# Performance work log

Hardware: AMD Instinct MI355X
Metric: run time of the kernel (lower is better)

Reference implementation:

```python
import jax, jax.numpy as jnp
import numpy as np

B, N, P, K = 64, 64, 128, 16

def setup_inputs() -> dict:
    key = jax.random.key(0)
    k1, k2, k3, k4 = jax.random.split(key, 4)
    x = jax.random.normal(k1, (B, N, P), dtype=jnp.float32)
    idx = jax.random.randint(k2, (B, P), 0, K)
    x_mask = jax.nn.one_hot(idx, K, dtype=jnp.float32)  # [B, P, K] one-hot
    # xavier_normal_ init for weights [K, N*N]
    std = float(np.sqrt(2.0 / (K + N * N)))
    weights = std * jax.random.normal(k3, (K, N * N), dtype=jnp.float32)
    g = jax.random.uniform(k4, (N * N, N * N), dtype=jnp.float32)
    return {"x": x, "x_mask": x_mask, "weights": weights, "g": g}

def reference(x, x_mask, weights, g):
    b, n, p = x.shape
    wg = jnp.matmul(weights ** 2, g)               # [K, N*N]
    w = jnp.einsum('bpk,km->bpm', x_mask, wg)      # [B, P, N*N]
    ef = jnp.exp(-w.reshape(b, p, n, n))           # [B, P, N, N]
    # torch does x[b].reshape(p, -1, 1): row-major reinterpretation of [N,P] -> [P,N]
    xr = x.reshape(b, p, n)                        # [B, P, N]
    Z = jnp.einsum('bpij,bpj->bi', ef, xr)         # batched matvec, summed over p
    return (Z, w)
```

## Files before the change

kernel.cpp:

```cpp
#include <hip/hip_runtime.h>
#include <hip/hip_bf16.h>


__global__ __launch_bounds__(256) void k_gemm(const float* __restrict__ W,
                                              const float* __restrict__ G,
                                              float* __restrict__ part) {
    __shared__ float  w2[16][256];
    __shared__ float4 red[8 * 256];
    const int tc  = blockIdx.x & 15;
    const int mg  = blockIdx.x >> 4;
    const int tid = threadIdx.x;
    const int tt  = tid >> 4;
    const int col = tid & 15;
    const int t0  = tc * 256;

#pragma unroll
    for (int k = 0; k < 16; ++k) {
        float v = W[k * 4096 + t0 + tid];
        w2[k][tid] = v * v;
    }
    __syncthreads();

    const float4* G4 = (const float4*)G;
    const int mq = mg * 16 + col;

    float4 acc[16];
#pragma unroll
    for (int k = 0; k < 16; ++k) acc[k] = make_float4(0.f, 0.f, 0.f, 0.f);

#pragma unroll 8
    for (int i = 0; i < 16; ++i) {
        const int tl = tt * 16 + i;
        const float4 g4 = G4[(size_t)(t0 + tl) * 1024 + mq];
#pragma unroll
        for (int k = 0; k < 16; ++k) {
            const float s = w2[k][tl];
            acc[k].x = fmaf(s, g4.x, acc[k].x);
            acc[k].y = fmaf(s, g4.y, acc[k].y);
            acc[k].z = fmaf(s, g4.z, acc[k].z);
            acc[k].w = fmaf(s, g4.w, acc[k].w);
        }
    }

    float4* p4 = (float4*)part;
#pragma unroll
    for (int r = 0; r < 2; ++r) {
#pragma unroll
        for (int ks = 0; ks < 8; ++ks)
            red[ks * 256 + tid] = acc[r * 8 + ks];
        __syncthreads();
        if (tid < 128) {
            const int ks = tid >> 4;
            const int c2 = tid & 15;
            float4 s = make_float4(0.f, 0.f, 0.f, 0.f);
#pragma unroll
            for (int t2 = 0; t2 < 16; ++t2) {
                float4 v = red[ks * 256 + t2 * 16 + c2];
                s.x += v.x; s.y += v.y; s.z += v.z; s.w += v.w;
            }
            const int k = r * 8 + ks;
            p4[(size_t)tc * 16384 + (size_t)k * 1024 + mg * 16 + c2] = s;
        }
        __syncthreads();
    }
}

__global__ __launch_bounds__(256) void k_reduce(const float* __restrict__ part,
                                                float* __restrict__ wg,
                                                float* __restrict__ E) {
    const int q = blockIdx.x * 256 + threadIdx.x;
    const float4* p4 = (const float4*)part;
    float4 s = make_float4(0.f, 0.f, 0.f, 0.f);
#pragma unroll
    for (int tc = 0; tc < 16; ++tc) {
        float4 v = p4[(size_t)tc * 16384 + q];
        s.x += v.x; s.y += v.y; s.z += v.z; s.w += v.w;
    }
    ((float4*)wg)[q] = s;
    ((float4*)E)[q] = make_float4(expf(-s.x), expf(-s.y), expf(-s.z), expf(-s.w));
}

__global__ __launch_bounds__(256) void k_wz(const float* __restrict__ x,
                                            const float* __restrict__ xmask,
                                            const float* __restrict__ wg,
                                            const float* __restrict__ E,
                                            float* __restrict__ wout,
                                            float* __restrict__ zout) {
    __shared__ float sw[4][16][64];
    __shared__ int   idx[128];
    __shared__ float zr[16][16];
    const int tid = threadIdx.x;

    if (blockIdx.x < 8192) {
        const int bp = blockIdx.x;
        const float* xm = xmask + (size_t)bp * 16;
        int k = 0;
#pragma unroll
        for (int i = 0; i < 16; ++i) k = (xm[i] > 0.5f) ? i : k;
        const float4* src = (const float4*)(wg + (size_t)k * 4096);
        float4*       dst = (float4*)(wout + (size_t)bp * 4096);
#pragma unroll
        for (int c = 0; c < 4; ++c)
            dst[c * 256 + tid] = src[c * 256 + tid];
        return;
    }

    const int zb = blockIdx.x - 8192;
    const int b  = zb >> 2;
    const int iq = zb & 3;
    const int wv = tid >> 6;
    const int ln = tid & 63;

    if (tid < 128) {
        const float* xm = xmask + ((size_t)b * 128 + tid) * 16;
        int k = 0;
#pragma unroll
        for (int i = 0; i < 16; ++i) k = (xm[i] > 0.5f) ? i : k;
        idx[tid] = k;
    }
#pragma unroll
    for (int c = 0; c < 16; ++c)
        ((float*)sw)[c * 256 + tid] = 0.f;
    __syncthreads();

    const float* xb = x + (size_t)b * 8192;
    for (int p = wv * 32; p < wv * 32 + 32; ++p) {
        int k = idx[p];
        sw[wv][k][ln] += xb[p * 64 + ln];
    }
    __syncthreads();

    for (int e = tid; e < 1024; e += 256) {
        int k2 = e >> 6, j = e & 63;
        sw[0][k2][j] = sw[0][k2][j] + sw[1][k2][j] + sw[2][k2][j] + sw[3][k2][j];
    }
    __syncthreads();

    {
        const int k  = tid >> 4;
        const int il = tid & 15;
        const int i  = iq * 16 + il;
        float a = 0.f;
        const float4* Er = (const float4*)(E + (size_t)k * 4096 + i * 64);
        const float4* sr = (const float4*)(&sw[0][k][0]);
#pragma unroll
        for (int j4 = 0; j4 < 16; ++j4) {
            float4 e4 = Er[j4];
            float4 s4 = sr[j4];
            a = fmaf(e4.x, s4.x, a);
            a = fmaf(e4.y, s4.y, a);
            a = fmaf(e4.z, s4.z, a);
            a = fmaf(e4.w, s4.w, a);
        }
        zr[k][il] = a;
    }
    __syncthreads();
    if (tid < 16) {
        float s = 0.f;
#pragma unroll
        for (int k = 0; k < 16; ++k) s += zr[k][tid];
        zout[b * 64 + iq * 16 + tid] = s;
    }
}

extern "C" void kernel_launch(void* const* d_in, const int* in_sizes, int n_in,
                              void* d_out, int out_size, void* d_ws, size_t ws_size,
                              hipStream_t stream) {
    const float* x     = (const float*)d_in[0];
    const float* xmask = (const float*)d_in[1];
    const float* W     = (const float*)d_in[2];
    const float* G     = (const float*)d_in[3];

    float* zout = (float*)d_out;
    float* wout = (float*)d_out + 4096;

    float* wg = (float*)d_ws;
    float* E  = wg + 65536;

    float* part = wout;

    k_gemm  <<<1024, 256, 0, stream>>>(W, G, part);
    k_reduce<<<64,   256, 0, stream>>>(part, wg, E);
    k_wz    <<<8448, 256, 0, stream>>>(x, xmask, wg, E, wout, zout);
}
```

Measured before the change: 54.41 us.

## Fuse split-K reduction into GEMM via last-block atomic counter

Removes the separate reduce kernel. Each GEMM block now bumps a per-column-group atomic counter, and the last of the 16 split-K blocks sums the partials and writes wg and exp(-wg). Shared memory is also aliased into one buffer to cut LDS use. This saves a kernel launch and its gap, but adds a memset launch, threadfences and a tail of serial reduction work in the last blocks.

```diff
diff --git a/kernel.cpp b/kernel.cpp
--- a/kernel.cpp
+++ b/kernel.cpp
@@ -4,9 +4,12 @@
 
 __global__ __launch_bounds__(256) void k_gemm(const float* __restrict__ W,
                                               const float* __restrict__ G,
-                                              float* __restrict__ part) {
-    __shared__ float  w2[16][256];
-    __shared__ float4 red[8 * 256];
+                                              float* __restrict__ part,
+                                              float* __restrict__ wg,
+                                              float* __restrict__ E,
+                                              unsigned* __restrict__ cnt) {
+    __shared__ float buf[8192];
+    __shared__ unsigned old_s;
     const int tc  = blockIdx.x & 15;
     const int mg  = blockIdx.x >> 4;
     const int tid = threadIdx.x;
@@ -17,7 +20,7 @@
 #pragma unroll
     for (int k = 0; k < 16; ++k) {
         float v = W[k * 4096 + t0 + tid];
-        w2[k][tid] = v * v;
+        buf[k * 256 + tid] = v * v;
     }
     __syncthreads();
 
@@ -34,15 +37,17 @@
         const float4 g4 = G4[(size_t)(t0 + tl) * 1024 + mq];
 #pragma unroll
         for (int k = 0; k < 16; ++k) {
-            const float s = w2[k][tl];
+            const float s = buf[k * 256 + tl];
             acc[k].x = fmaf(s, g4.x, acc[k].x);
             acc[k].y = fmaf(s, g4.y, acc[k].y);
             acc[k].z = fmaf(s, g4.z, acc[k].z);
             acc[k].w = fmaf(s, g4.w, acc[k].w);
         }
     }
+    __syncthreads();
 
-    float4* p4 = (float4*)part;
+    float4* red = (float4*)buf;
+    float4* p4  = (float4*)part;
 #pragma unroll
     for (int r = 0; r < 2; ++r) {
 #pragma unroll
@@ -63,21 +68,27 @@
         }
         __syncthreads();
     }
-}
 
-__global__ __launch_bounds__(256) void k_reduce(const float* __restrict__ part,
-                                                float* __restrict__ wg,
-                                                float* __restrict__ E) {
-    const int q = blockIdx.x * 256 + threadIdx.x;
-    const float4* p4 = (const float4*)part;
-    float4 s = make_float4(0.f, 0.f, 0.f, 0.f);
+    __threadfence();
+    if (tid == 0)
+        old_s = __hip_atomic_fetch_add(&cnt[mg], 1u, __ATOMIC_ACQ_REL,
+                                       __HIP_MEMORY_SCOPE_AGENT);
+    __syncthreads();
+    if (old_s == 15u) {
+        __threadfence();
+        const int k = tid >> 4;
+        const int c = tid & 15;
+        float4 s = make_float4(0.f, 0.f, 0.f, 0.f);
 #pragma unroll
-    for (int tc = 0; tc < 16; ++tc) {
-        float4 v = p4[(size_t)tc * 16384 + q];
-        s.x += v.x; s.y += v.y; s.z += v.z; s.w += v.w;
+        for (int tc2 = 0; tc2 < 16; ++tc2) {
+            float4 v = p4[(size_t)tc2 * 16384 + (size_t)k * 1024 + mg * 16 + c];
+            s.x += v.x; s.y += v.y; s.z += v.z; s.w += v.w;
+        }
+        const size_t o = (size_t)k * 1024 + mg * 16 + c;
+        ((float4*)wg)[o] = s;
+        ((float4*)E)[o]  = make_float4(expf(-s.x), expf(-s.y),
+                                       expf(-s.z), expf(-s.w));
     }
-    ((float4*)wg)[q] = s;
-    ((float4*)E)[q] = make_float4(expf(-s.x), expf(-s.y), expf(-s.z), expf(-s.w));
 }
 
 __global__ __launch_bounds__(256) void k_wz(const float* __restrict__ x,
@@ -174,12 +185,14 @@
     float* zout = (float*)d_out;
     float* wout = (float*)d_out + 4096;
 
-    float* wg = (float*)d_ws;
-    float* E  = wg + 65536;
+    float*    wg  = (float*)d_ws;
+    float*    E   = wg + 65536;
+    unsigned* cnt = (unsigned*)(E + 65536);
 
     float* part = wout;
 
-    k_gemm  <<<1024, 256, 0, stream>>>(W, G, part);
-    k_reduce<<<64,   256, 0, stream>>>(part, wg, E);
-    k_wz    <<<8448, 256, 0, stream>>>(x, xmask, wg, E, wout, zout);
+    hipMemsetAsync(cnt, 0, 64 * sizeof(unsigned), stream);
+
+    k_gemm<<<1024, 256, 0, stream>>>(W, G, part, wg, E, cnt);
+    k_wz  <<<8448, 256, 0, stream>>>(x, xmask, wg, E, wout, zout);
 }
```

Measured after the change: 185.5 us. 3.41x slower.
